# Kernel tuning notes

Hardware: AMD Instinct MI355X
Metric: run time of the kernel (lower is better)

Reference implementation:

```python
import jax, jax.numpy as jnp
import numpy as np

NS = (128, 128, 128)       # ns_mesh
NODES = 4                  # interpolation_nodes (P3M, even -> floor-based indexing)
N_POINTS = 100000
N_CHANNELS = 8
BOX = 10.0


def _weights_p3m4(x):
    # x: (P, 3) relative offsets in [-1/2, 1/2]; returns (4, P, 3)
    x2 = x * x
    x3 = x * x2
    c = jnp.asarray(1.0 / 48.0, dtype=x.dtype)
    return jnp.stack([
        c * (1 - 6 * x + 12 * x2 - 8 * x3),
        c * (23 - 30 * x - 12 * x2 + 24 * x3),
        c * (23 + 30 * x - 12 * x2 - 24 * x3),
        c * (1 + 6 * x + 12 * x2 + 8 * x3),
    ])


def setup_inputs() -> dict:
    key = jax.random.key(0)
    k1, k2 = jax.random.split(key)
    positions = jax.random.uniform(k1, (N_POINTS, 3), dtype=jnp.float32) * BOX
    particle_weights = jax.random.normal(k2, (N_POINTS, N_CHANNELS), dtype=jnp.float32)
    cell = jnp.eye(3, dtype=jnp.float32) * BOX
    return {"positions": positions, "particle_weights": particle_weights, "cell": cell}


def reference(positions, particle_weights, cell):
    nx, ny, nz = NS
    ns_f = jnp.array(NS, dtype=positions.dtype)
    inv_cell = jnp.linalg.inv(cell)

    # --- compute_weights ---
    pos_rel = ns_f * (positions @ inv_cell)        # (P,3) mesh-scaled fractional coords
    idx0 = jnp.floor(pos_rel)                      # even nodes -> floor of position
    offsets = pos_rel - (idx0 + 0.5)               # in [-1/2, 1/2]
    w = _weights_p3m4(offsets)                     # (4, P, 3) per-axis 1d weights
    shifts = jnp.arange(1 - (NODES + 1) // 2, 1 + NODES // 2, dtype=jnp.int32)  # [-1,0,1,2]
    ns_i = jnp.array(NS, dtype=jnp.int32)
    idx = (idx0.astype(jnp.int32)[None] + shifts[:, None, None]) % ns_i  # (4,P,3) periodic
    xi, yi, zi = idx[..., 0], idx[..., 1], idx[..., 2]  # (4,P) each

    # 3D outer product of per-axis weights: (4,4,4,P)
    w3 = w[:, None, None, :, 0] * w[None, :, None, :, 1] * w[None, None, :, :, 2]
    # flattened mesh index per (i,j,k,point): (4,4,4,P)
    lin = (xi[:, None, None] * ny + yi[None, :, None]) * nz + zi[None, None, :]

    # --- points_to_mesh: scatter-add weighted charges onto mesh ---
    C = particle_weights.shape[1]
    vals = w3[..., None] * particle_weights        # (4,4,4,P,C)
    rho_flat = jnp.zeros((nx * ny * nz, C), dtype=positions.dtype)
    rho_flat = rho_flat.at[lin.reshape(-1)].add(vals.reshape(-1, C))

    # --- mesh_to_points: gather mesh values back to particle positions ---
    gathered = rho_flat[lin]                       # (4,4,4,P,C)
    out = jnp.sum(gathered * w3[..., None], axis=(0, 1, 2))  # (P,C)
    return out
```

## Files before the change

### kernel.cpp

```cpp
#include <hip/hip_runtime.h>

static constexpr int NXC   = 128;
static constexpr int NPTS  = 100000;
static constexpr int NCH   = 8;
static constexpr int TS    = 8;
static constexpr int NT    = 16;
static constexpr int NTILES = NT * NT * NT;
static constexpr int SLOT  = 64;
static constexpr int REC   = 20;
static constexpr int CMAX  = 320;
static constexpr int OMAX  = SLOT;
static constexpr int NMAX  = 48;

static constexpr int M1   = 1 | (1 << 10) | (1 << 20);
static constexpr int M7   = 7 * M1;
static constexpr int M8   = 8 | (8 << 10) | (8 << 20);
static constexpr int M120 = 120 | (120 << 10) | (120 << 20);

__device__ __forceinline__ void axis_weights(float x, float w[4]) {
    float x2 = x * x, x3 = x2 * x;
    const float c = 1.0f / 48.0f;
    w[0] = c * (1.0f  - 6.0f  * x + 12.0f * x2 - 8.0f  * x3);
    w[1] = c * (23.0f - 30.0f * x - 12.0f * x2 + 24.0f * x3);
    w[2] = c * (23.0f + 30.0f * x - 12.0f * x2 - 24.0f * x3);
    w[3] = c * (1.0f  + 6.0f  * x + 12.0f * x2 + 8.0f  * x3);
}

__device__ __forceinline__ void mesh_coords(const float* __restrict__ pos,
                                            const float* __restrict__ cell,
                                            int p, float& rx, float& ry, float& rz) {
    float a = cell[0], b = cell[1], c = cell[2];
    float d = cell[3], e = cell[4], f = cell[5];
    float g = cell[6], h = cell[7], i9 = cell[8];
    float c00 = e * i9 - f * h, c01 = f * g - d * i9, c02 = d * h - e * g;
    float c10 = c * h - b * i9, c11 = a * i9 - c * g, c12 = b * g - a * h;
    float c20 = b * f - c * e,  c21 = c * d - a * f,  c22 = a * e - b * d;
    float det = a * c00 + b * c01 + c * c02;
    float s = 128.0f / det;
    float p0 = pos[p * 3 + 0], p1 = pos[p * 3 + 1], p2 = pos[p * 3 + 2];
    rx = s * (p0 * c00 + p1 * c01 + p2 * c02);
    ry = s * (p0 * c10 + p1 * c11 + p2 * c12);
    rz = s * (p0 * c20 + p1 * c21 + p2 * c22);
}

__global__ __launch_bounds__(256) void bin_k(const float* __restrict__ pos,
                                             const float* __restrict__ pw,
                                             const float* __restrict__ cell,
                                             int* __restrict__ cursor,
                                             int* __restrict__ scell,
                                             int* __restrict__ spid,
                                             float* __restrict__ srec) {
    int p = blockIdx.x * 256 + threadIdx.x;
    if (p >= NPTS) return;
    float rx, ry, rz;
    mesh_coords(pos, cell, p, rx, ry, rz);
    float fx = floorf(rx), fy = floorf(ry), fz = floorf(rz);
    int ix = ((int)fx) & (NXC - 1), iy = ((int)fy) & (NXC - 1), iz = ((int)fz) & (NXC - 1);
    int tile = ((ix >> 3) * NT + (iy >> 3)) * NT + (iz >> 3);
    int slot = atomicAdd(cursor + tile, 1);
    if (slot >= SLOT) return;
    int idx = tile * SLOT + slot;
    scell[idx] = ix | (iy << 10) | (iz << 20);
    spid[idx] = p;
    float wx[4], wy[4], wz[4];
    axis_weights(rx - fx - 0.5f, wx);
    axis_weights(ry - fy - 0.5f, wy);
    axis_weights(rz - fz - 0.5f, wz);
    float4* r = reinterpret_cast<float4*>(srec) + (size_t)idx * 5;
    r[0] = make_float4(wx[0], wx[1], wx[2], wx[3]);
    r[1] = make_float4(wy[0], wy[1], wy[2], wy[3]);
    r[2] = make_float4(wz[0], wz[1], wz[2], wz[3]);
    const float4* pw4 = reinterpret_cast<const float4*>(pw + (size_t)p * NCH);
    r[3] = pw4[0];
    r[4] = pw4[1];
}

__device__ __forceinline__ float corr4(float4 wp, float4 wq, int d) {
    float s0 = d == 0 ? wq.x : d == -1 ? wq.y : d == -2 ? wq.z : d == -3 ? wq.w : 0.0f;
    float s1 = d == 1 ? wq.x : d ==  0 ? wq.y : d == -1 ? wq.z : d == -2 ? wq.w : 0.0f;
    float s2 = d == 2 ? wq.x : d ==  1 ? wq.y : d ==  0 ? wq.z : d == -1 ? wq.w : 0.0f;
    float s3 = d == 3 ? wq.x : d ==  2 ? wq.y : d ==  1 ? wq.z : d ==  0 ? wq.w : 0.0f;
    return wp.x * s0 + wp.y * s1 + wp.z * s2 + wp.w * s3;
}

__global__ __launch_bounds__(256) void pair_k(const int* __restrict__ cursor,
                                              const int* __restrict__ scell,
                                              const int* __restrict__ spid,
                                              const float* __restrict__ srec,
                                              float* __restrict__ out) {
    __shared__ int ccell[CMAX];
    __shared__ int cidx[CMAX];
    __shared__ int nlist[OMAX * NMAX];
    __shared__ int cnt[OMAX];
    __shared__ int ncand;

    int b = blockIdx.x;
    int tx = b >> 8, ty = (b >> 4) & 15, tz = b & 15;
    int tid = threadIdx.x;
    int lane = tid & 63;
    int nown = min(cursor[b], SLOT);
    if (nown == 0) return;
    int begin = b * SLOT;

    if (tid == 0) ncand = 0;
    for (int i = tid; i < OMAX; i += 256) cnt[i] = 0;
    __syncthreads();

    int crew = tid >> 3, cl = tid & 7;
    int base_x = tx * TS - 3, base_y = ty * TS - 3, base_z = tz * TS - 3;
    if (crew < 27) {
        int ox = crew / 9 - 1, oy = (crew / 3) % 3 - 1, oz = crew % 3 - 1;
        int nt = ((((tx + ox) & 15) * NT + ((ty + oy) & 15)) * NT) + ((tz + oz) & 15);
        int n0 = nt * SLOT;
        int cn = min(cursor[nt], SLOT);
        unsigned long long crewmask = 0xFFull << ((crew & 7) * 8);
        for (int s0 = 0; s0 < cn; s0 += 8) {
            int s = s0 + cl;
            bool pass = false;
            int i = 0, c = 0;
            if (s < cn) {
                i = n0 + s;
                c = scell[i];
                pass = (((c & 1023)         - base_x) & 127) < 14
                    && ((((c >> 10) & 1023) - base_y) & 127) < 14
                    && ((((c >> 20) & 1023) - base_z) & 127) < 14;
            }
            unsigned long long m = __ballot(pass) & crewmask;
            int kb = 0;
            if (cl == 0 && m) kb = atomicAdd(&ncand, __popcll(m));
            kb = __shfl(kb, lane & 56, 64);
            if (pass) {
                int k = kb + __popcll(m & ((1ull << lane) - 1ull));
                if (k < CMAX) { ccell[k] = c; cidx[k] = i; }
            }
        }
    }
    __syncthreads();
    int nc = min(ncand, CMAX);

    int sub = tid & 7, pg = tid >> 3;

    for (int p0 = 0; p0 < nown; p0 += 32) {
        int p = p0 + pg;
        bool live = p < nown;
        int bias = 0;
        if (live) {
            int pc = scell[begin + p];
            int px = pc & 1023, py = (pc >> 10) & 1023, pz = (pc >> 20) & 1023;
            bias = ((131 - px) & 127) | (((131 - py) & 127) << 10)
                 | (((131 - pz) & 127) << 20);
        }
        for (int j0 = 0; j0 < nc; j0 += 8) {
            int j = j0 + sub;
            if (live && j < nc) {
                int t = ccell[j] + bias;
                if (((t & M120) == 0) && ((((t & M7) + M1) & M8) == 0)) {
                    int ent = (cidx[j] << 9) | ((t & 7) << 6)
                            | (((t >> 10) & 7) << 3) | ((t >> 20) & 7);
                    int slot = atomicAdd(&cnt[p], 1);
                    if (slot < NMAX) nlist[p * NMAX + slot] = ent;
                }
            }
        }
    }
    __syncthreads();

    const float4* recs = reinterpret_cast<const float4*>(srec);
    for (int p0 = 0; p0 < nown; p0 += 32) {
        int p = p0 + pg;
        bool live = p < nown;
        int n = 0;
        float4 pxw, pyw, pzw;
        if (live) {
            n = min(cnt[p], NMAX);
            const float4* r = recs + (size_t)(begin + p) * 5;
            pxw = r[0]; pyw = r[1]; pzw = r[2];
        }
        float acc[8] = {0, 0, 0, 0, 0, 0, 0, 0};
        for (int s = sub; s < n; s += 8) {
            int ent = nlist[p * NMAX + s];
            const float4* q = recs + (size_t)(ent >> 9) * 5;
            int dx = ((ent >> 6) & 7) - 3;
            int dy = ((ent >> 3) & 7) - 3;
            int dz = (ent & 7) - 3;
            float4 qxw = q[0], qyw = q[1], qzw = q[2];
            float S = corr4(pxw, qxw, dx) * corr4(pyw, qyw, dy) * corr4(pzw, qzw, dz);
            float4 ch0 = q[3], ch1 = q[4];
            acc[0] += S * ch0.x; acc[1] += S * ch0.y;
            acc[2] += S * ch0.z; acc[3] += S * ch0.w;
            acc[4] += S * ch1.x; acc[5] += S * ch1.y;
            acc[6] += S * ch1.z; acc[7] += S * ch1.w;
        }
        #pragma unroll
        for (int m = 1; m <= 4; m <<= 1) {
            #pragma unroll
            for (int c = 0; c < 8; ++c) acc[c] += __shfl_xor(acc[c], m, 64);
        }
        if (live && sub == 0) {
            int pid = spid[begin + p];
            float4* o = reinterpret_cast<float4*>(out + (size_t)pid * NCH);
            o[0] = make_float4(acc[0], acc[1], acc[2], acc[3]);
            o[1] = make_float4(acc[4], acc[5], acc[6], acc[7]);
        }
    }
}

extern "C" void kernel_launch(void* const* d_in, const int* in_sizes, int n_in,
                              void* d_out, int out_size, void* d_ws, size_t ws_size,
                              hipStream_t stream) {
    const float* pos  = (const float*)d_in[0];
    const float* pw   = (const float*)d_in[1];
    const float* cell = (const float*)d_in[2];
    float* out = (float*)d_out;

    int*   cursor = (int*)d_ws;
    int*   scell  = cursor + NTILES;
    int*   spid   = scell + NTILES * SLOT;
    float* srec   = (float*)(spid + NTILES * SLOT);

    hipMemsetAsync(cursor, 0, NTILES * sizeof(int), stream);

    int pblocks = (NPTS + 255) / 256;
    bin_k<<<pblocks, 256, 0, stream>>>(pos, pw, cell, cursor, scell, spid, srec);
    pair_k<<<NTILES, 256, 0, stream>>>(cursor, scell, spid, srec, out);
}
```

Baseline: 70.40 us.

## Bin halo candidates into x-slabs and scan only the relevant slab range

Candidate particles from neighboring tiles are bucketed into 14 x-slabs in shared memory, then compacted by prefix offsets. Each owned particle scans only the 7 slabs within its x interaction range instead of all candidates. Neighbor-list slot assignment now uses wave ballots instead of shared atomics. This cuts the pair-test work per particle but adds two extra barriers and a compaction pass, and it silently drops any candidates beyond 32 per slab.

Result: faster. 63.33 us (-10.0%).

```diff
diff --git a/kernel.cpp b/kernel.cpp
--- a/kernel.cpp
+++ b/kernel.cpp
@@ -8,14 +8,10 @@
 static constexpr int NTILES = NT * NT * NT;
 static constexpr int SLOT  = 64;
 static constexpr int REC   = 20;
-static constexpr int CMAX  = 320;
+static constexpr int SLABCAP = 32;
+static constexpr int AMAX  = 14 * SLABCAP;
 static constexpr int OMAX  = SLOT;
 static constexpr int NMAX  = 48;
-
-static constexpr int M1   = 1 | (1 << 10) | (1 << 20);
-static constexpr int M7   = 7 * M1;
-static constexpr int M8   = 8 | (8 << 10) | (8 << 20);
-static constexpr int M120 = 120 | (120 << 10) | (120 << 20);
 
 __device__ __forceinline__ void axis_weights(float x, float w[4]) {
     float x2 = x * x, x3 = x2 * x;
@@ -88,11 +84,14 @@
                                               const int* __restrict__ spid,
                                               const float* __restrict__ srec,
                                               float* __restrict__ out) {
-    __shared__ int ccell[CMAX];
-    __shared__ int cidx[CMAX];
+    __shared__ int slabA[AMAX];
+    __shared__ int slabB[AMAX];
+    __shared__ int A1[AMAX];
+    __shared__ int A2[AMAX];
     __shared__ int nlist[OMAX * NMAX];
     __shared__ int cnt[OMAX];
-    __shared__ int ncand;
+    __shared__ int scnt[14];
+    __shared__ int soff[15];
 
     int b = blockIdx.x;
     int tx = b >> 8, ty = (b >> 4) & 15, tz = b & 15;
@@ -102,7 +101,7 @@
     if (nown == 0) return;
     int begin = b * SLOT;
 
-    if (tid == 0) ncand = 0;
+    if (tid < 14) scnt[tid] = 0;
     for (int i = tid; i < OMAX; i += 256) cnt[i] = 0;
     __syncthreads();
 
@@ -113,55 +112,84 @@
         int nt = ((((tx + ox) & 15) * NT + ((ty + oy) & 15)) * NT) + ((tz + oz) & 15);
         int n0 = nt * SLOT;
         int cn = min(cursor[nt], SLOT);
-        unsigned long long crewmask = 0xFFull << ((crew & 7) * 8);
         for (int s0 = 0; s0 < cn; s0 += 8) {
             int s = s0 + cl;
-            bool pass = false;
-            int i = 0, c = 0;
             if (s < cn) {
-                i = n0 + s;
-                c = scell[i];
-                pass = (((c & 1023)         - base_x) & 127) < 14
-                    && ((((c >> 10) & 1023) - base_y) & 127) < 14
-                    && ((((c >> 20) & 1023) - base_z) & 127) < 14;
+                int i = n0 + s;
+                int c = scell[i];
+                int lcx = ((c & 1023) - base_x) & 127;
+                int lcy = (((c >> 10) & 1023) - base_y) & 127;
+                int lcz = (((c >> 20) & 1023) - base_z) & 127;
+                if (lcx < 14 && lcy < 14 && lcz < 14) {
+                    int slot = atomicAdd(&scnt[lcx], 1);
+                    if (slot < SLABCAP) {
+                        slabA[lcx * SLABCAP + slot] = lcy | (lcz << 5) | (lcx << 10);
+                        slabB[lcx * SLABCAP + slot] = i;
+                    }
+                }
             }
-            unsigned long long m = __ballot(pass) & crewmask;
-            int kb = 0;
-            if (cl == 0 && m) kb = atomicAdd(&ncand, __popcll(m));
-            kb = __shfl(kb, lane & 56, 64);
-            if (pass) {
-                int k = kb + __popcll(m & ((1ull << lane) - 1ull));
-                if (k < CMAX) { ccell[k] = c; cidx[k] = i; }
-            }
-        }
-    }
-    __syncthreads();
-    int nc = min(ncand, CMAX);
+        }
+    }
+    __syncthreads();
+    if (tid == 0) {
+        int run = 0;
+        #pragma unroll
+        for (int s2 = 0; s2 < 14; ++s2) {
+            soff[s2] = run;
+            run += min(scnt[s2], SLABCAP);
+        }
+        soff[14] = run;
+    }
+    __syncthreads();
+    for (int u = tid; u < AMAX; u += 256) {
+        int s2 = u >> 5, i2 = u & (SLABCAP - 1);
+        if (i2 < min(scnt[s2], SLABCAP)) {
+            int d = soff[s2] + i2;
+            A1[d] = slabA[u];
+            A2[d] = slabB[u];
+        }
+    }
+    __syncthreads();
 
     int sub = tid & 7, pg = tid >> 3;
 
     for (int p0 = 0; p0 < nown; p0 += 32) {
         int p = p0 + pg;
         bool live = p < nown;
-        int bias = 0;
+        int lpx = 0, lpyh = 0, lpzh = 0, jbeg = 0, span = 0;
         if (live) {
             int pc = scell[begin + p];
-            int px = pc & 1023, py = (pc >> 10) & 1023, pz = (pc >> 20) & 1023;
-            bias = ((131 - px) & 127) | (((131 - py) & 127) << 10)
-                 | (((131 - pz) & 127) << 20);
-        }
-        for (int j0 = 0; j0 < nc; j0 += 8) {
-            int j = j0 + sub;
-            if (live && j < nc) {
-                int t = ccell[j] + bias;
-                if (((t & M120) == 0) && ((((t & M7) + M1) & M8) == 0)) {
-                    int ent = (cidx[j] << 9) | ((t & 7) << 6)
-                            | (((t >> 10) & 7) << 3) | ((t >> 20) & 7);
-                    int slot = atomicAdd(&cnt[p], 1);
-                    if (slot < NMAX) nlist[p * NMAX + slot] = ent;
+            lpx  = (pc & 1023) - tx * TS;
+            lpyh = ((pc >> 10) & 1023) - ty * TS + 3;
+            lpzh = ((pc >> 20) & 1023) - tz * TS + 3;
+            jbeg = soff[lpx];
+            span = soff[lpx + 7] - jbeg;
+        }
+        int creg = 0;
+        for (int j0 = 0; __any(j0 < span); j0 += 8) {
+            bool pass = (j0 + sub) < span;
+            int a1 = 0, j = jbeg + j0 + sub;
+            if (pass) {
+                a1 = A1[j];
+                int dy3 = (a1 & 31) - lpyh + 3;
+                int dz3 = ((a1 >> 5) & 31) - lpzh + 3;
+                pass = ((unsigned)dy3 <= 6u) && ((unsigned)dz3 <= 6u);
+            }
+            unsigned long long m = __ballot(pass);
+            int mg = (int)(m >> (lane & 56)) & 255;
+            if (pass) {
+                int slot = creg + __popc(mg & ((1 << sub) - 1));
+                if (slot < NMAX) {
+                    int dxp3 = ((a1 >> 10) & 15) - lpx;
+                    int dy3 = (a1 & 31) - lpyh + 3;
+                    int dz3 = ((a1 >> 5) & 31) - lpzh + 3;
+                    int ent = (A2[j] << 9) | (dxp3 << 6) | (dy3 << 3) | dz3;
+                    nlist[p * NMAX + slot] = ent;
                 }
             }
-        }
+            creg += __popc(mg);
+        }
+        if (live && sub == 0) cnt[p] = creg;
     }
     __syncthreads();
 
```
